# Performance work log

Measured on AMD Instinct MI355X. Metric: run time of the kernel, lower is better.

## Reference

```python
import jax, jax.numpy as jnp
import numpy as np

N, L, S = 2, 3000, 3000
C = 256          # in_depth
H = 256          # hidden_depth
FC = 8           # heads_count
SC_HID = H // FC # per-head dim of projected features
SCALE = (C // FC) ** 0.5  # torch code uses sc = in_depth // heads_count for scaling


def setup_inputs() -> dict:
    key = jax.random.key(0)
    ks = jax.random.split(key, 7)
    x0 = jax.random.normal(ks[0], (N, L, C), jnp.float32)
    x1 = jax.random.normal(ks[1], (N, S, C), jnp.float32)
    mask = jax.random.bernoulli(ks[2], 0.9, (N, L, S))
    W_proj = jax.random.normal(ks[3], (C, 2 * H), jnp.float32) / np.sqrt(C).astype(np.float32)
    b_proj = jax.random.normal(ks[4], (2 * H,), jnp.float32) * 0.01
    W_merge = jax.random.normal(ks[5], (H, C), jnp.float32) / np.sqrt(H).astype(np.float32)
    b_merge = jax.random.normal(ks[6], (C,), jnp.float32) * 0.01
    return {"x0": x0, "x1": x1, "mask": mask,
            "W_proj": W_proj, "b_proj": b_proj,
            "W_merge": W_merge, "b_merge": b_merge}


def _split_heads(x, W_proj, b_proj):
    # x: [n, t, C] -> proj [n, t, 2H] -> (qk, v) each [n, fc, t, sc]
    n, t, _ = x.shape
    p = (x @ W_proj + b_proj).reshape(n, t, 2, FC, SC_HID)  # layout (k fc sc)
    qk = jnp.transpose(p[:, :, 0], (0, 2, 1, 3))
    v = jnp.transpose(p[:, :, 1], (0, 2, 1, 3))
    return qk, v


def reference(x0, x1, mask, W_proj, b_proj, W_merge, b_merge):
    q0, v0 = _split_heads(x0, W_proj, b_proj)  # [n, f, l, d]
    q1, v1 = _split_heads(x1, W_proj, b_proj)  # [n, f, s, d]

    sim = jnp.einsum('nfld,nfsd->nfls', q0, q1)            # full score matrix
    sim = jnp.where(mask[:, None], sim, -jnp.inf) / SCALE  # mask then scale (as in torch)

    a01 = jnp.nan_to_num(jax.nn.softmax(sim, axis=3))  # rows over s
    a10 = jnp.nan_to_num(jax.nn.softmax(sim, axis=2))  # rows over l (== softmax(sim^T, -1))

    m0 = jnp.einsum('nfls,nfsd->nfld', a01, v1)  # [n, f, l, d]
    m1 = jnp.einsum('nfls,nfld->nfsd', a10, v0)  # [n, f, s, d]

    m0 = jnp.transpose(m0, (0, 2, 1, 3)).reshape(m0.shape[0], L, H) @ W_merge + b_merge
    m1 = jnp.transpose(m1, (0, 2, 1, 3)).reshape(m1.shape[0], S, H) @ W_merge + b_merge
    return m0, m1
```

## Files before the change

kernel.cpp:

```cpp
#include <hip/hip_runtime.h>
#include <cstdint>
#include <cstddef>

typedef unsigned int u32;
typedef unsigned short u16;
typedef uint8_t u8;
typedef unsigned long long u64;

constexpr int kNB = 2, kL = 3000, kS = 3000, kC = 256, kH = 256, kFC = 8, kD = 32;
constexpr int kTP = 3008;
constexpr int kMW = 48;
constexpr float kQSC = 0.5050097568f;

typedef __attribute__((ext_vector_type(8))) short short8;
typedef __attribute__((ext_vector_type(4))) float f32x4;

__device__ __forceinline__ u16 f2bf(float f) {
  u32 u = __float_as_uint(f);
  u += 0x7FFFu + ((u >> 16) & 1u);
  return (u16)(u >> 16);
}
__device__ __forceinline__ float bf2f(u16 h) { return __uint_as_float(((u32)h) << 16); }
__device__ __forceinline__ f32x4 mfma16(short8 a, short8 b, f32x4 c) {
  return __builtin_amdgcn_mfma_f32_16x16x32_bf16(a, b, c, 0, 0, 0);
}
__device__ __forceinline__ u32 pk2(float a, float b) {
  return (__float_as_uint(a) >> 16) | (__float_as_uint(b) & 0xFFFF0000u);
}
__device__ __forceinline__ u32 bytes_nz(u32 w) {
  return ((w & 0xFFu) ? 1u : 0u) | (((w >> 8) & 0xFFu) ? 2u : 0u)
       | (((w >> 16) & 0xFFu) ? 4u : 0u) | ((w >> 24) ? 8u : 0u);
}
__device__ __forceinline__ u32 h2_nz(u32 w) {
  return ((w & 0xFFFFu) ? 1u : 0u) | ((w >> 16) ? 2u : 0u);
}

constexpr size_t SZ_Q   = (size_t)kNB * kFC * kTP * kD * 2;
constexpr size_t SZ_MH  = (size_t)kNB * kTP * kH * 2;
constexpr size_t SZ_XB  = (size_t)kNB * kL * kC * 2;
constexpr size_t SZ_MKB = (size_t)kNB * kTP * kMW * 8;
constexpr size_t OFF_Q0 = 256;
constexpr size_t OFF_Q1 = OFF_Q0 + SZ_Q;
constexpr size_t OFF_V0 = OFF_Q1 + SZ_Q;
constexpr size_t OFF_V1 = OFF_V0 + SZ_Q;
constexpr size_t OFF_M0 = OFF_V1 + SZ_Q;
constexpr size_t OFF_M1 = OFF_M0 + SZ_MH;
constexpr size_t OFF_WT = OFF_M1 + SZ_MH;
constexpr size_t OFF_WM = OFF_WT + (size_t)2 * kH * kC * 2;
constexpr size_t OFF_X0 = OFF_WM + (size_t)kC * kH * 2;
constexpr size_t OFF_X1 = OFF_X0 + SZ_XB;
constexpr size_t OFF_MKB  = OFF_X1 + SZ_XB;
constexpr size_t OFF_MKBT = OFF_MKB + SZ_MKB;

__global__ __launch_bounds__(256) void k_detect(const u8* __restrict__ mraw,
                                                const u8* __restrict__ xraw,
                                                u32* __restrict__ flag) {
  __shared__ int c1[4], c3f[4], c3c, cexp;
  int tid = threadIdx.x;
  if (tid < 4) { c1[tid] = 0; c3f[tid] = 0; }
  if (tid == 0) { c3c = 0; cexp = 0; }
  __syncthreads();
  int l1[4] = {0,0,0,0}, l3f[4] = {0,0,0,0}, l3c = 0, lex = 0;
  for (int j = 0; j < 16; ++j) {
    int i = tid * 16 + j;
    u8 b = mraw[i];
    int r = i & 3;
    l1[r]  += (b == 1);
    l3f[r] += (b == 0x3F);
    if (i & 1) l3c += (b == 0x3C);
    if (r == 1) { u32 v = xraw[i] & 0x7F; lex += (v >= 0x3E && v <= 0x40); }
  }
  for (int r = 0; r < 4; ++r) {
    if (l1[r])  atomicAdd(&c1[r], l1[r]);
    if (l3f[r]) atomicAdd(&c3f[r], l3f[r]);
  }
  if (l3c) atomicAdd(&c3c, l3c);
  if (lex) atomicAdd(&cexp, lex);
  __syncthreads();
  if (tid == 0) {
    u32 mf;
    if (c1[1] + c1[2] + c1[3] > 64) mf = 0;
    else if (c1[0] > 64)            mf = 2;
    else if (c3f[1] > 64)           mf = 1;
    else if (c3c > 64)              mf = 4;
    else                            mf = 3;
    flag[0] = mf;
    flag[1] = (cexp > 300) ? 0u : 1u;
  }
}

constexpr int NB_MASK = 47 * 47 * 2;
constexpr int NB_CVT  = 3000;
constexpr int NB_WT   = 2 * kH + kC;

__global__ __launch_bounds__(256) void k_prep(const void* __restrict__ mraw,
                                              const void* __restrict__ x0,
                                              const void* __restrict__ x1,
                                              const void* __restrict__ Wp,
                                              const void* __restrict__ Wm,
                                              const u32* __restrict__ flag,
                                              u64* __restrict__ mkb, u64* __restrict__ mkbt,
                                              u16* __restrict__ xb0, u16* __restrict__ xb1,
                                              u16* __restrict__ WT, u16* __restrict__ WmT) {
  const int bx = blockIdx.x, tid = threadIdx.x;
  if (bx < NB_MASK) {
    const u32 mf = flag[0];
    const int n = bx / 2209, r2 = bx % 2209;
    const int l0 = (r2 / 47) * 64, s0 = (r2 % 47) * 64;
    __shared__ u16 tb[64][4];
    {
      const int row = tid >> 2, sg = (tid & 3) * 16;
      const int l = l0 + row;
      u32 bits = 0;
      if (l < kL) {
        const size_t base = ((size_t)n * kL + l) * kS + s0 + sg;
        const bool full = (s0 + sg + 16 <= kS);
        if (mf == 3) {
          if (full) {
            const float4* p = (const float4*)(((const float*)mraw) + base);
            float4 a = p[0], b = p[1], c = p[2], d = p[3];
            bits = (u32)(a.x != 0.f)        | ((u32)(a.y != 0.f) << 1)
                 | ((u32)(a.z != 0.f) << 2) | ((u32)(a.w != 0.f) << 3)
                 | ((u32)(b.x != 0.f) << 4) | ((u32)(b.y != 0.f) << 5)
                 | ((u32)(b.z != 0.f) << 6) | ((u32)(b.w != 0.f) << 7)
                 | ((u32)(c.x != 0.f) << 8) | ((u32)(c.y != 0.f) << 9)
                 | ((u32)(c.z != 0.f) << 10)| ((u32)(c.w != 0.f) << 11)
                 | ((u32)(d.x != 0.f) << 12)| ((u32)(d.y != 0.f) << 13)
                 | ((u32)(d.z != 0.f) << 14)| ((u32)(d.w != 0.f) << 15);
          } else {
            for (int i = 0; i < 16; ++i)
              if (s0 + sg + i < kS && ((const float*)mraw)[base + i] != 0.f) bits |= 1u << i;
          }
        } else if (mf == 2) {
          if (full) {
            const uint4* p = (const uint4*)(((const u32*)mraw) + base);
            uint4 a = p[0], b = p[1], c = p[2], d = p[3];
            bits = (u32)(a.x != 0)        | ((u32)(a.y != 0) << 1)
                 | ((u32)(a.z != 0) << 2) | ((u32)(a.w != 0) << 3)
                 | ((u32)(b.x != 0) << 4) | ((u32)(b.y != 0) << 5)
                 | ((u32)(b.z != 0) << 6) | ((u32)(b.w != 0) << 7)
                 | ((u32)(c.x != 0) << 8) | ((u32)(c.y != 0) << 9)
                 | ((u32)(c.z != 0) << 10)| ((u32)(c.w != 0) << 11)
                 | ((u32)(d.x != 0) << 12)| ((u32)(d.y != 0) << 13)
                 | ((u32)(d.z != 0) << 14)| ((u32)(d.w != 0) << 15);
          } else {
            for (int i = 0; i < 16; ++i)
              if (s0 + sg + i < kS && ((const u32*)mraw)[base + i]) bits |= 1u << i;
          }
        } else if (mf == 0) {
          if (full) {
            const u8* m8 = (const u8*)mraw + base;
            uint2 a = *(const uint2*)(m8);
            uint2 b = *(const uint2*)(m8 + 8);
            bits = bytes_nz(a.x) | (bytes_nz(a.y) << 4)
                 | (bytes_nz(b.x) << 8) | (bytes_nz(b.y) << 12);
          } else {
            for (int i = 0; i < 16; ++i)
              if (s0 + sg + i < kS && ((const u8*)mraw)[base + i]) bits |= 1u << i;
          }
        } else {
          if (full) {
            const u16* m16 = (const u16*)mraw + base;
            uint4 a = *(const uint4*)(m16);
            uint4 b = *(const uint4*)(m16 + 8);
            bits = h2_nz(a.x) | (h2_nz(a.y) << 2) | (h2_nz(a.z) << 4) | (h2_nz(a.w) << 6)
                 | (h2_nz(b.x) << 8) | (h2_nz(b.y) << 10)
                 | (h2_nz(b.z) << 12) | (h2_nz(b.w) << 14);
          } else {
            for (int i = 0; i < 16; ++i)
              if (s0 + sg + i < kS && ((const u16*)mraw)[base + i]) bits |= 1u << i;
          }
        }
      }
      tb[row][tid & 3] = (u16)bits;
    }
    __syncthreads();
    const int w = tid >> 6, lane = tid & 63;
    for (int k = 0; k < 16; ++k) {
      const int ro = w * 16 + k;
      u32 b1 = (tb[ro][lane >> 4] >> (lane & 15)) & 1;
      u64 word = __ballot((int)b1);
      if (lane == 0) mkb[((size_t)n * kTP + l0 + ro) * kMW + (s0 >> 6)] = word;
      u32 b2 = (tb[lane][ro >> 4] >> (ro & 15)) & 1;
      u64 wordt = __ballot((int)b2);
      if (lane == 0) mkbt[((size_t)n * kTP + s0 + ro) * kMW + (l0 >> 6)] = wordt;
    }
  } else if (bx < NB_MASK + NB_CVT) {
    const u32 f2 = flag[1];
    const int b2 = bx - NB_MASK;
    const void* X = (b2 >= 1500) ? x1 : x0;
    u16* B = (b2 >= 1500) ? xb1 : xb0;
    const int i = (b2 % 1500) * 256 + tid;
    if (f2 == 0) {
      ((uint2*)B)[i] = ((const uint2*)X)[i];
    } else {
      float4 v = ((const float4*)X)[i];
      uint2 o;
      o.x = (u32)f2bf(v.x) | ((u32)f2bf(v.y) << 16);
      o.y = (u32)f2bf(v.z) | ((u32)f2bf(v.w) << 16);
      ((uint2*)B)[i] = o;
    }
  } else {
    const u32 f2 = flag[1];
    const int b = bx - NB_MASK - NB_CVT, k = tid;
    if (b < 2 * kH) {
      int col = b;
      u16 v = (f2 == 0) ? ((const u16*)Wp)[(size_t)k * (2 * kH) + col]
                        : f2bf(((const float*)Wp)[(size_t)k * (2 * kH) + col]);
      WT[(size_t)col * kC + k] = v;
    } else {
      int col = b - 2 * kH;
      u16 v = (f2 == 0) ? ((const u16*)Wm)[(size_t)k * kC + col]
                        : f2bf(((const float*)Wm)[(size_t)k * kC + col]);
      WmT[(size_t)col * kH + k] = v;
    }
  }
}

__global__ __launch_bounds__(256) void k_proj(const u16* __restrict__ xb0,
                                              const u16* __restrict__ xb1,
                                              const u16* __restrict__ WT,
                                              const void* __restrict__ bias,
                                              const u32* __restrict__ flag,
                                              u16* __restrict__ q0, u16* __restrict__ v0t,
                                              u16* __restrict__ q1, u16* __restrict__ v1t) {
  const u32 f2 = flag[1];
  const int z = blockIdx.z;
  const u16* X = z ? xb1 : xb0;
  u16* Q = z ? q1 : q0;
  u16* V = z ? v1t : v0t;
  const int tid = threadIdx.x, w = tid >> 6, lane = tid & 63;
  const int quad = lane >> 4, c16 = lane & 15;
  const int rb = blockIdx.x, cb = blockIdx.y;

  __align__(16) __shared__ u16 sB[64 * 264];
  {
    const u16* wp = WT + (size_t)(cb * 64 + (tid >> 2)) * kC + (tid & 3) * 64;
    u16* sp = sB + (tid >> 2) * 264 + (tid & 3) * 64;
#pragma unroll
    for (int i = 0; i < 8; ++i) *(uint4*)(sp + i * 8) = *(const uint4*)(wp + i * 8);
  }
  __syncthreads();

  const int arow = rb * 64 + w * 16 + c16;
  const u16* ap = X + (size_t)arow * kC + quad * 8;
  f32x4 acc[4];
#pragma unroll
  for (int cg = 0; cg < 4; ++cg) acc[cg] = f32x4{0.f,0.f,0.f,0.f};
#pragma unroll
  for (int k0 = 0; k0 < 8; ++k0) {
    short8 a = *(const short8*)(ap + k0 * 32);
#pragma unroll
    for (int cg = 0; cg < 4; ++cg) {
      short8 b = *(const short8*)(sB + (cg * 16 + c16) * 264 + k0 * 32 + quad * 8);
      acc[cg] = mfma16(a, b, acc[cg]);
    }
  }

  const int row0 = rb * 64 + w * 16 + quad * 4;
  if (row0 < 6000) {
    const int n = (row0 >= kL) ? 1 : 0;
    const int t0 = row0 - n * kL;
#pragma unroll
    for (int cg = 0; cg < 4; ++cg) {
      const int c = cb * 64 + cg * 16 + c16;
      float bb = (f2 == 0) ? bf2f(((const u16*)bias)[c]) : ((const float*)bias)[c];
      if (c < kH) {
        int ff = c >> 5, d = c & 31;
        u16* qp = Q + ((size_t)(n * kFC + ff) * kTP + t0) * kD + d;
#pragma unroll
        for (int r = 0; r < 4; ++r) qp[(size_t)r * kD] = f2bf((acc[cg][r] + bb) * kQSC);
      } else {
        int cc = c - kH;
        int ff = cc >> 5, d = cc & 31;
        uint2 o;
        o.x = (u32)f2bf(acc[cg][0] + bb) | ((u32)f2bf(acc[cg][1] + bb) << 16);
        o.y = (u32)f2bf(acc[cg][2] + bb) | ((u32)f2bf(acc[cg][3] + bb) << 16);
        *(uint2*)(V + ((size_t)(n * kFC + ff) * kD + d) * kTP + t0) = o;
      }
    }
  }
}

__global__ __launch_bounds__(128, 1) void k_flash(const u16* __restrict__ q0,
                                                  const u16* __restrict__ q1,
                                                  const u16* __restrict__ v0t,
                                                  const u16* __restrict__ v1t,
                                                  const u64* __restrict__ mkb,
                                                  const u64* __restrict__ mkbt,
                                                  u16* __restrict__ m0h, u16* __restrict__ m1h) {
  const int z = blockIdx.z;
  const u16* QA = z ? q1 : q0;
  const u16* QB = z ? q0 : q1;
  const u16* VT = z ? v0t : v1t;
  const u64* MB = z ? mkbt : mkb;
  u16* MO = z ? m1h : m0h;

  const int nf = blockIdx.y, n = nf >> 3, f = nf & 7;
  const int tid = threadIdx.x, w = tid >> 6, lane = tid & 63;
  const int quad = lane >> 4, c16 = lane & 15;

  __align__(16) __shared__ float sBuf[8 * 9 * 64];
  u16* sP = (u16*)sBuf + w * 2 * (16 * 72);

  const u16* qa = QA + (size_t)(n * kFC + f) * kTP * kD;
  const u16* qb = QB + (size_t)(n * kFC + f) * kTP * kD;
  const u16* vt = VT + (size_t)(n * kFC + f) * kD * kTP;
  const u64* mb = MB + (size_t)n * kTP * kMW;

  const int l0 = blockIdx.x * 128;

  short8 af[8];
  int rc[8];
#pragma unroll
  for (int g = 0; g < 8; ++g) {
    int ra = l0 + g * 16 + c16;
    rc[g] = (ra > kTP - 1) ? (kTP - 1) : ra;
    af[g] = *(const short8*)(qa + (size_t)rc[g] * kD + quad * 8);
  }

  f32x4 acc[8][2];
  float pSum[8];
#pragma unroll
  for (int g = 0; g < 8; ++g) {
    acc[g][0] = f32x4{0.f,0.f,0.f,0.f};
    acc[g][1] = f32x4{0.f,0.f,0.f,0.f};
    pSum[g] = 0.f;
  }

  const int jc0 = w * 24;
  const int nch = w ? 23 : 24;
  uint4 mq[8];

#pragma unroll 1
  for (int jcl = 0; jcl < nch; ++jcl) {
    const int jc = jc0 + jcl;
    if ((jcl & 1) == 0) {
#pragma unroll
      for (int g = 0; g < 8; ++g)
        mq[g] = *(const uint4*)(mb + (size_t)rc[g] * kMW + jc);
    }
    const int j0 = jc * 64;
    const u16* qbase = qb + (size_t)(j0 + c16) * kD + quad * 8;
    short8 aq0 = *(const short8*)(qbase);
    short8 aq1 = *(const short8*)(qbase + (size_t)16 * kD);
    short8 aq2 = *(const short8*)(qbase + (size_t)32 * kD);
    short8 aq3 = *(const short8*)(qbase + (size_t)48 * kD);
    const u16* vb = vt + (size_t)c16 * kTP + j0 + quad * 8;
    short8 bv00 = *(const short8*)(vb);
    short8 bv01 = *(const short8*)(vb + (size_t)16 * kTP);
    short8 bv10 = *(const short8*)(vb + 32);
    short8 bv11 = *(const short8*)(vb + (size_t)16 * kTP + 32);

#pragma unroll
    for (int g = 0; g < 8; ++g) {
      const u32 lo = (jcl & 1) ? mq[g].z : mq[g].x;
      const u32 hi = (jcl & 1) ? mq[g].w : mq[g].y;
      u16* Pt = sP + (g & 1) * (16 * 72);
      float ps = 0.f;
#pragma unroll
      for (int t = 0; t < 4; ++t) {
        short8 aq = (t == 0) ? aq0 : (t == 1) ? aq1 : (t == 2) ? aq2 : aq3;
        f32x4 zz = {0.f,0.f,0.f,0.f};
        f32x4 s = mfma16(aq, af[g], zz);
        const u32 hh = (t & 2) ? hi : lo;
        const int base = (t & 1) * 16 + quad * 4;
        float p0 = ((hh >> (base + 0)) & 1) ? __builtin_amdgcn_exp2f(s[0]) : 0.f;
        float p1 = ((hh >> (base + 1)) & 1) ? __builtin_amdgcn_exp2f(s[1]) : 0.f;
        float p2 = ((hh >> (base + 2)) & 1) ? __builtin_amdgcn_exp2f(s[2]) : 0.f;
        float p3 = ((hh >> (base + 3)) & 1) ? __builtin_amdgcn_exp2f(s[3]) : 0.f;
        ps += (p0 + p1) + (p2 + p3);
        uint2 pw; pw.x = pk2(p0, p1); pw.y = pk2(p2, p3);
        *(uint2*)(Pt + c16 * 72 + t * 16 + quad * 4) = pw;
      }
      pSum[g] += ps;
      short8 ap0 = *(const short8*)(Pt + c16 * 72 + quad * 8);
      short8 ap1 = *(const short8*)(Pt + c16 * 72 + 32 + quad * 8);
      acc[g][0] = mfma16(ap0, bv00, acc[g][0]);
      acc[g][1] = mfma16(ap0, bv01, acc[g][1]);
      acc[g][0] = mfma16(ap1, bv10, acc[g][0]);
      acc[g][1] = mfma16(ap1, bv11, acc[g][1]);
    }
  }

#pragma unroll
  for (int g = 0; g < 8; ++g) {
    float s = pSum[g];
    s += __shfl_xor(s, 16);
    s += __shfl_xor(s, 32);
    pSum[g] = s;
  }

  __syncthreads();
  if (w == 1) {
#pragma unroll
    for (int g = 0; g < 8; ++g) {
#pragma unroll
      for (int r = 0; r < 4; ++r) {
        sBuf[(g * 9 + r)     * 64 + lane] = acc[g][0][r];
        sBuf[(g * 9 + 4 + r) * 64 + lane] = acc[g][1][r];
      }
      sBuf[(g * 9 + 8) * 64 + lane] = pSum[g];
    }
  }
  __syncthreads();
  if (w == 0) {
#pragma unroll
    for (int g = 0; g < 8; ++g) {
      float lsum = pSum[g] + sBuf[(g * 9 + 8) * 64 + lane];
#pragma unroll
      for (int r = 0; r < 4; ++r) {
        float n0 = acc[g][0][r] + sBuf[(g * 9 + r)     * 64 + lane];
        float n1 = acc[g][1][r] + sBuf[(g * 9 + 4 + r) * 64 + lane];
        float ls = __shfl(lsum, quad * 4 + r);
        float rd = (ls > 0.f) ? (1.f / ls) : 0.f;
        int lrow = l0 + g * 16 + quad * 4 + r;
        if (lrow < kL) {
          size_t basep = ((size_t)n * kTP + lrow) * kH + f * kD;
          MO[basep + c16]      = f2bf(n0 * rd);
          MO[basep + 16 + c16] = f2bf(n1 * rd);
        }
      }
    }
  }
}

__global__ __launch_bounds__(256) void k_merge(const u16* __restrict__ m0h,
                                               const u16* __restrict__ m1h,
                                               const u16* __restrict__ WmT,
                                               const void* __restrict__ bias,
                                               const u32* __restrict__ flag,
                                               void* __restrict__ out) {
  const u32 f2 = flag[1];
  const int z = blockIdx.z;
  const u16* A = z ? m1h : m0h;
  const int tid = threadIdx.x, w = tid >> 6, lane = tid & 63;
  const int quad = lane >> 4, c16 = lane & 15;
  const int rb = blockIdx.x, cb = blockIdx.y;

  __align__(16) __shared__ u16 sB[64 * 264];
  {
    const u16* wp = WmT + (size_t)(cb * 64 + (tid >> 2)) * kH + (tid & 3) * 64;
    u16* sp = sB + (tid >> 2) * 264 + (tid & 3) * 64;
#pragma unroll
    for (int i = 0; i < 8; ++i) *(uint4*)(sp + i * 8) = *(const uint4*)(wp + i * 8);
  }
  __syncthreads();

  const int arow = rb * 64 + w * 16 + c16;
  const u16* ap = A + (size_t)arow * kH + quad * 8;
  f32x4 acc[4];
#pragma unroll
  for (int cg = 0; cg < 4; ++cg) acc[cg] = f32x4{0.f,0.f,0.f,0.f};
#pragma unroll
  for (int k0 = 0; k0 < 8; ++k0) {
    short8 a = *(const short8*)(ap + k0 * 32);
#pragma unroll
    for (int cg = 0; cg < 4; ++cg) {
      short8 b = *(const short8*)(sB + (cg * 16 + c16) * 264 + k0 * 32 + quad * 8);
      acc[cg] = mfma16(a, b, acc[cg]);
    }
  }

  const int row0 = rb * 64 + w * 16 + quad * 4;
  const int n = (row0 >= kTP) ? 1 : 0;
  const int t0 = row0 - n * kTP;
  const size_t obase = (size_t)z * ((size_t)kNB * kL * kC);
#pragma unroll
  for (int cg = 0; cg < 4; ++cg) {
    const int c = cb * 64 + cg * 16 + c16;
    float bb = (f2 == 0) ? bf2f(((const u16*)bias)[c]) : ((const float*)bias)[c];
#pragma unroll
    for (int r = 0; r < 4; ++r) {
      const int t = t0 + r;
      if (t < kL) {
        size_t oi = obase + ((size_t)n * kL + t) * kC + c;
        float v = acc[cg][r] + bb;
        if (f2 == 0) ((u16*)out)[oi] = f2bf(v);
        else         ((float*)out)[oi] = v;
      }
    }
  }
}

extern "C" void kernel_launch(void* const* d_in, const int* in_sizes, int n_in,
                              void* d_out, int out_size, void* d_ws, size_t ws_size,
                              hipStream_t stream) {
  (void)in_sizes; (void)n_in; (void)out_size; (void)ws_size;
  u8* ws = (u8*)d_ws;
  u32* flag = (u32*)ws;
  u16* q0  = (u16*)(ws + OFF_Q0);
  u16* q1  = (u16*)(ws + OFF_Q1);
  u16* v0t = (u16*)(ws + OFF_V0);
  u16* v1t = (u16*)(ws + OFF_V1);
  u16* m0h = (u16*)(ws + OFF_M0);
  u16* m1h = (u16*)(ws + OFF_M1);
  u16* WT  = (u16*)(ws + OFF_WT);
  u16* WmT = (u16*)(ws + OFF_WM);
  u16* xb0 = (u16*)(ws + OFF_X0);
  u16* xb1 = (u16*)(ws + OFF_X1);
  u64* mkb  = (u64*)(ws + OFF_MKB);
  u64* mkbt = (u64*)(ws + OFF_MKBT);

  const void* x0 = d_in[0];
  const void* x1 = d_in[1];
  const void* mraw = d_in[2];
  const void* Wp = d_in[3];
  const void* bp = d_in[4];
  const void* Wm = d_in[5];
  const void* bm = d_in[6];

  k_detect<<<1, 256, 0, stream>>>((const u8*)mraw, (const u8*)x0, flag);
  k_prep<<<dim3(NB_MASK + NB_CVT + NB_WT), 256, 0, stream>>>(
      mraw, x0, x1, Wp, Wm, flag, mkb, mkbt, xb0, xb1, WT, WmT);
  k_proj<<<dim3(94, 8, 2), 256, 0, stream>>>(xb0, xb1, WT, bp, flag, q0, v0t, q1, v1t);
  k_flash<<<dim3(24, 16, 2), 128, 0, stream>>>(q0, q1, v0t, v1t, mkb, mkbt, m0h, m1h);
  k_merge<<<dim3(94, 4, 2), 256, 0, stream>>>(m0h, m1h, WmT, bm, flag, d_out);
}
```

Measured before the change: 303.8 us.

## Inline dtype detection into kernels and retile flash kernel to 4 warps, 64 rows

Removes the separate single-block detect kernel. Each block now recomputes the mask and input dtype flags from a small sample, which saves one launch and its serial dependency. The flash kernel moves from 128 threads over 128 query rows to 256 threads over 64 query rows. Its key chunks are split across 4 warps, the bitmask is stored column-major and fetched one word per lane with shuffles, and the 4 warp partials are reduced through shared memory. The row sum now uses bf16-truncated probabilities so it matches the values fed to the MFMA. In exchange, every block does redundant detection work with extra barriers, and the final reduction across warps grows.

New measurement: 255.2 us. -16.0%, faster.

```diff
diff --git a/kernel.cpp b/kernel.cpp
--- a/kernel.cpp
+++ b/kernel.cpp
@@ -27,6 +27,9 @@
 __device__ __forceinline__ u32 pk2(float a, float b) {
   return (__float_as_uint(a) >> 16) | (__float_as_uint(b) & 0xFFFF0000u);
 }
+__device__ __forceinline__ float truncbf(float a) {
+  return __uint_as_float(__float_as_uint(a) & 0xFFFF0000u);
+}
 __device__ __forceinline__ u32 bytes_nz(u32 w) {
   return ((w & 0xFFu) ? 1u : 0u) | (((w >> 8) & 0xFFu) ? 2u : 0u)
        | (((w >> 16) & 0xFFu) ? 4u : 0u) | ((w >> 24) ? 8u : 0u);
@@ -35,10 +38,60 @@
   return ((w & 0xFFFFu) ? 1u : 0u) | ((w >> 16) ? 2u : 0u);
 }
 
+__device__ __forceinline__ u32 detect_mf_block(const u8* __restrict__ mraw,
+                                               int tid, int* cnt) {
+  if (tid < 8) cnt[tid] = 0;
+  __syncthreads();
+  uint4 mv = ((const uint4*)mraw)[tid];
+  u32 wds[4] = {mv.x, mv.y, mv.z, mv.w};
+  int l1[4] = {0,0,0,0}; int l3f1 = 0, l3c = 0;
+#pragma unroll
+  for (int k = 0; k < 4; ++k) {
+    u32 wv = wds[k];
+#pragma unroll
+    for (int j = 0; j < 4; ++j) {
+      u32 b = (wv >> (8 * j)) & 0xFFu;
+      l1[j] += (b == 1u);
+      if (j == 1) l3f1 += (b == 0x3Fu);
+      if (j & 1) l3c += (b == 0x3Cu);
+    }
+  }
+  if (l1[0]) atomicAdd(&cnt[0], l1[0]);
+  if (l1[1]) atomicAdd(&cnt[1], l1[1]);
+  if (l1[2]) atomicAdd(&cnt[2], l1[2]);
+  if (l1[3]) atomicAdd(&cnt[3], l1[3]);
+  if (l3f1)  atomicAdd(&cnt[4], l3f1);
+  if (l3c)   atomicAdd(&cnt[5], l3c);
+  __syncthreads();
+  u32 mf;
+  if (cnt[1] + cnt[2] + cnt[3] > 64) mf = 0;
+  else if (cnt[0] > 64)              mf = 2;
+  else if (cnt[4] > 64)              mf = 1;
+  else if (cnt[5] > 64)              mf = 4;
+  else                               mf = 3;
+  return mf;
+}
+__device__ __forceinline__ u32 detect_f2_block(const u8* __restrict__ xraw,
+                                               int tid, int* cnt) {
+  if (tid == 0) cnt[0] = 0;
+  __syncthreads();
+  uint4 xv = ((const uint4*)xraw)[tid];
+  u32 wds[4] = {xv.x, xv.y, xv.z, xv.w};
+  int lex = 0;
+#pragma unroll
+  for (int k = 0; k < 4; ++k) {
+    u32 b = (wds[k] >> 8) & 0x7Fu;
+    lex += (b >= 0x3Eu && b <= 0x40u);
+  }
+  if (lex) atomicAdd(&cnt[0], lex);
+  __syncthreads();
+  return (cnt[0] > 300) ? 0u : 1u;
+}
+
 constexpr size_t SZ_Q   = (size_t)kNB * kFC * kTP * kD * 2;
 constexpr size_t SZ_MH  = (size_t)kNB * kTP * kH * 2;
 constexpr size_t SZ_XB  = (size_t)kNB * kL * kC * 2;
-constexpr size_t SZ_MKB = (size_t)kNB * kTP * kMW * 8;
+constexpr size_t SZ_MKB = (size_t)kNB * kMW * kTP * 8;
 constexpr size_t OFF_Q0 = 256;
 constexpr size_t OFF_Q1 = OFF_Q0 + SZ_Q;
 constexpr size_t OFF_V0 = OFF_Q1 + SZ_Q;
@@ -52,43 +105,6 @@
 constexpr size_t OFF_MKB  = OFF_X1 + SZ_XB;
 constexpr size_t OFF_MKBT = OFF_MKB + SZ_MKB;
 
-__global__ __launch_bounds__(256) void k_detect(const u8* __restrict__ mraw,
-                                                const u8* __restrict__ xraw,
-                                                u32* __restrict__ flag) {
-  __shared__ int c1[4], c3f[4], c3c, cexp;
-  int tid = threadIdx.x;
-  if (tid < 4) { c1[tid] = 0; c3f[tid] = 0; }
-  if (tid == 0) { c3c = 0; cexp = 0; }
-  __syncthreads();
-  int l1[4] = {0,0,0,0}, l3f[4] = {0,0,0,0}, l3c = 0, lex = 0;
-  for (int j = 0; j < 16; ++j) {
-    int i = tid * 16 + j;
-    u8 b = mraw[i];
-    int r = i & 3;
-    l1[r]  += (b == 1);
-    l3f[r] += (b == 0x3F);
-    if (i & 1) l3c += (b == 0x3C);
-    if (r == 1) { u32 v = xraw[i] & 0x7F; lex += (v >= 0x3E && v <= 0x40); }
-  }
-  for (int r = 0; r < 4; ++r) {
-    if (l1[r])  atomicAdd(&c1[r], l1[r]);
-    if (l3f[r]) atomicAdd(&c3f[r], l3f[r]);
-  }
-  if (l3c) atomicAdd(&c3c, l3c);
-  if (lex) atomicAdd(&cexp, lex);
-  __syncthreads();
-  if (tid == 0) {
-    u32 mf;
-    if (c1[1] + c1[2] + c1[3] > 64) mf = 0;
-    else if (c1[0] > 64)            mf = 2;
-    else if (c3f[1] > 64)           mf = 1;
-    else if (c3c > 64)              mf = 4;
-    else                            mf = 3;
-    flag[0] = mf;
-    flag[1] = (cexp > 300) ? 0u : 1u;
-  }
-}
-
 constexpr int NB_MASK = 47 * 47 * 2;
 constexpr int NB_CVT  = 3000;
 constexpr int NB_WT   = 2 * kH + kC;
@@ -98,13 +114,13 @@
                                               const void* __restrict__ x1,
                                               const void* __restrict__ Wp,
                                               const void* __restrict__ Wm,
-                                              const u32* __restrict__ flag,
                                               u64* __restrict__ mkb, u64* __restrict__ mkbt,
                                               u16* __restrict__ xb0, u16* __restrict__ xb1,
                                               u16* __restrict__ WT, u16* __restrict__ WmT) {
   const int bx = blockIdx.x, tid = threadIdx.x;
+  __shared__ int dcnt[8];
   if (bx < NB_MASK) {
-    const u32 mf = flag[0];
+    const u32 mf = detect_mf_block((const u8*)mraw, tid, dcnt);
     const int n = bx / 2209, r2 = bx % 2209;
     const int l0 = (r2 / 47) * 64, s0 = (r2 % 47) * 64;
     __shared__ u16 tb[64][4];
@@ -180,13 +196,13 @@
       const int ro = w * 16 + k;
       u32 b1 = (tb[ro][lane >> 4] >> (lane & 15)) & 1;
       u64 word = __ballot((int)b1);
-      if (lane == 0) mkb[((size_t)n * kTP + l0 + ro) * kMW + (s0 >> 6)] = word;
+      if (lane == 0) mkb[((size_t)n * kMW + (s0 >> 6)) * kTP + l0 + ro] = word;
       u32 b2 = (tb[lane][ro >> 4] >> (ro & 15)) & 1;
       u64 wordt = __ballot((int)b2);
-      if (lane == 0) mkbt[((size_t)n * kTP + s0 + ro) * kMW + (l0 >> 6)] = wordt;
+      if (lane == 0) mkbt[((size_t)n * kMW + (l0 >> 6)) * kTP + s0 + ro] = wordt;
     }
   } else if (bx < NB_MASK + NB_CVT) {
-    const u32 f2 = flag[1];
+    const u32 f2 = detect_f2_block((const u8*)x0, tid, dcnt);
     const int b2 = bx - NB_MASK;
     const void* X = (b2 >= 1500) ? x1 : x0;
     u16* B = (b2 >= 1500) ? xb1 : xb0;
@@ -201,7 +217,7 @@
       ((uint2*)B)[i] = o;
     }
   } else {
-    const u32 f2 = flag[1];
+    const u32 f2 = detect_f2_block((const u8*)x0, tid, dcnt);
     const int b = bx - NB_MASK - NB_CVT, k = tid;
     if (b < 2 * kH) {
       int col = b;
@@ -221,15 +237,17 @@
                                               const u16* __restrict__ xb1,
                                               const u16* __restrict__ WT,
                                               const void* __restrict__ bias,
-                                              const u32* __restrict__ flag,
+                                              const void* __restrict__ x0raw,
                                               u16* __restrict__ q0, u16* __restrict__ v0t,
                                               u16* __restrict__ q1, u16* __restrict__ v1t) {
-  const u32 f2 = flag[1];
+  __shared__ int dcnt[8];
+  const int tid = threadIdx.x;
+  const u32 f2 = detect_f2_block((const u8*)x0raw, tid, dcnt);
   const int z = blockIdx.z;
   const u16* X = z ? xb1 : xb0;
   u16* Q = z ? q1 : q0;
   u16* V = z ? v1t : v0t;
-  const int tid = threadIdx.x, w = tid >> 6, lane = tid & 63;
+  const int w = tid >> 6, lane = tid & 63;
   const int quad = lane >> 4, c16 = lane & 15;
   const int rb = blockIdx.x, cb = blockIdx.y;
 
@@ -282,13 +300,13 @@
   }
 }
 
-__global__ __launch_bounds__(128, 1) void k_flash(const u16* __restrict__ q0,
-                                                  const u16* __restrict__ q1,
-                                                  const u16* __restrict__ v0t,
-                                                  const u16* __restrict__ v1t,
-                                                  const u64* __restrict__ mkb,
-                                                  const u64* __restrict__ mkbt,
-                                                  u16* __restrict__ m0h, u16* __restrict__ m1h) {
+__global__ __launch_bounds__(256) void k_flash(const u16* __restrict__ q0,
+                                               const u16* __restrict__ q1,
+                                               const u16* __restrict__ v0t,
+                                               const u16* __restrict__ v1t,
+                                               const u64* __restrict__ mkb,
+                                               const u64* __restrict__ mkbt,
+                                               u16* __restrict__ m0h, u16* __restrict__ m1h) {
   const int z = blockIdx.z;
   const u16* QA = z ? q1 : q0;
   const u16* QB = z ? q0 : q1;
@@ -300,47 +318,36 @@
   const int tid = threadIdx.x, w = tid >> 6, lane = tid & 63;
   const int quad = lane >> 4, c16 = lane & 15;
 
-  __align__(16) __shared__ float sBuf[8 * 9 * 64];
-  u16* sP = (u16*)sBuf + w * 2 * (16 * 72);
+  __align__(16) __shared__ u16 sPall[4 * 4704];
+  u16* sP = sPall + w * 4704;
 
   const u16* qa = QA + (size_t)(n * kFC + f) * kTP * kD;
   const u16* qb = QB + (size_t)(n * kFC + f) * kTP * kD;
   const u16* vt = VT + (size_t)(n * kFC + f) * kD * kTP;
-  const u64* mb = MB + (size_t)n * kTP * kMW;
-
-  const int l0 = blockIdx.x * 128;
-
-  short8 af[8];
-  int rc[8];
-#pragma unroll
-  for (int g = 0; g < 8; ++g) {
-    int ra = l0 + g * 16 + c16;
-    rc[g] = (ra > kTP - 1) ? (kTP - 1) : ra;
-    af[g] = *(const short8*)(qa + (size_t)rc[g] * kD + quad * 8);
-  }
-
-  f32x4 acc[8][2];
-  float pSum[8];
-#pragma unroll
-  for (int g = 0; g < 8; ++g) {
+  const u64* mb = MB + (size_t)n * kMW * kTP;
+
+  const int l0 = blockIdx.x * 64;
+
+  short8 af[4];
+#pragma unroll
+  for (int g = 0; g < 4; ++g) {
+    const int ra = l0 + g * 16 + c16;
+    af[g] = *(const short8*)(qa + (size_t)ra * kD + quad * 8);
+  }
+
+  f32x4 acc[4][2];
+  float pSum[4];
+#pragma unroll
+  for (int g = 0; g < 4; ++g) {
     acc[g][0] = f32x4{0.f,0.f,0.f,0.f};
     acc[g][1] = f32x4{0.f,0.f,0.f,0.f};
     pSum[g] = 0.f;
   }
 
-  const int jc0 = w * 24;
-  const int nch = w ? 23 : 24;
-  uint4 mq[8];
-
 #pragma unroll 1
-  for (int jcl = 0; jcl < nch; ++jcl) {
-    const int jc = jc0 + jcl;
-    if ((jcl & 1) == 0) {
-#pragma unroll
-      for (int g = 0; g < 8; ++g)
-        mq[g] = *(const uint4*)(mb + (size_t)rc[g] * kMW + jc);
-    }
+  for (int jc = w; jc < 47; jc += 4) {
     const int j0 = jc * 64;
+    u64 mword = mb[(size_t)jc * kTP + l0 + lane];
     const u16* qbase = qb + (size_t)(j0 + c16) * kD + quad * 8;
     short8 aq0 = *(const short8*)(qbase);
     short8 aq1 = *(const short8*)(qbase + (size_t)16 * kD);
@@ -351,12 +358,12 @@
     short8 bv01 = *(const short8*)(vb + (size_t)16 * kTP);
     short8 bv10 = *(const short8*)(vb + 32);
     short8 bv11 = *(const short8*)(vb + (size_t)16 * kTP + 32);
-
-#pragma unroll
-    for (int g = 0; g < 8; ++g) {
-      const u32 lo = (jcl & 1) ? mq[g].z : mq[g].x;
-      const u32 hi = (jcl & 1) ? mq[g].w : mq[g].y;
-      u16* Pt = sP + (g & 1) * (16 * 72);
+    const u32 mlo = (u32)mword, mhi = (u32)(mword >> 32);
+
+#pragma unroll
+    for (int g = 0; g < 4; ++g) {
+      const u32 lo = (u32)__shfl((int)mlo, g * 16 + c16);
+      const u32 hi = (u32)__shfl((int)mhi, g * 16 + c16);
       float ps = 0.f;
 #pragma unroll
       for (int t = 0; t < 4; ++t) {
@@ -369,13 +376,13 @@
         float p1 = ((hh >> (base + 1)) & 1) ? __builtin_amdgcn_exp2f(s[1]) : 0.f;
         float p2 = ((hh >> (base + 2)) & 1) ? __builtin_amdgcn_exp2f(s[2]) : 0.f;
         float p3 = ((hh >> (base + 3)) & 1) ? __builtin_amdgcn_exp2f(s[3]) : 0.f;
-        ps += (p0 + p1) + (p2 + p3);
+        ps += (truncbf(p0) + truncbf(p1)) + (truncbf(p2) + truncbf(p3));
         uint2 pw; pw.x = pk2(p0, p1); pw.y = pk2(p2, p3);
-        *(uint2*)(Pt + c16 * 72 + t * 16 + quad * 4) = pw;
+        *(uint2*)(sP + (g * 16 + c16) * 72 + t * 16 + quad * 4) = pw;
       }
       pSum[g] += ps;
-      short8 ap0 = *(const short8*)(Pt + c16 * 72 + quad * 8);
-      short8 ap1 = *(const short8*)(Pt + c16 * 72 + 32 + quad * 8);
+      short8 ap0 = *(const short8*)(sP + (g * 16 + c16) * 72 + quad * 8);
+      short8 ap1 = *(const short8*)(sP + (g * 16 + c16) * 72 + 32 + quad * 8);
       acc[g][0] = mfma16(ap0, bv00, acc[g][0]);
       acc[g][1] = mfma16(ap0, bv01, acc[g][1]);
       acc[g][0] = mfma16(ap1, bv10, acc[g][0]);
@@ -384,7 +391,7 @@
   }
 
 #pragma unroll
-  for (int g = 0; g < 8; ++g) {
+  for (int g = 0; g < 4; ++g) {
     float s = pSum[g];
     s += __shfl_xor(s, 16);
     s += __shfl_xor(s, 32);
@@ -392,26 +399,34 @@
   }
 
   __syncthreads();
-  if (w == 1) {
-#pragma unroll
-    for (int g = 0; g < 8; ++g) {
+  float* buf = (float*)sPall;
+  if (w > 0) {
+    const int rbase = (w - 1) * 2304;
+#pragma unroll
+    for (int g = 0; g < 4; ++g) {
 #pragma unroll
       for (int r = 0; r < 4; ++r) {
-        sBuf[(g * 9 + r)     * 64 + lane] = acc[g][0][r];
-        sBuf[(g * 9 + 4 + r) * 64 + lane] = acc[g][1][r];
+        buf[rbase + (g * 9 + r)     * 64 + lane] = acc[g][0][r];
+        buf[rbase + (g * 9 + 4 + r) * 64 + lane] = acc[g][1][r];
       }
-      sBuf[(g * 9 + 8) * 64 + lane] = pSum[g];
+      buf[rbase + (g * 9 + 8) * 64 + lane] = pSum[g];
     }
   }
   __syncthreads();
   if (w == 0) {
 #pragma unroll
-    for (int g = 0; g < 8; ++g) {
-      float lsum = pSum[g] + sBuf[(g * 9 + 8) * 64 + lane];
+    for (int g = 0; g < 4; ++g) {
+      float lsum = pSum[g];
+#pragma unroll
+      for (int ww = 0; ww < 3; ++ww) lsum += buf[ww * 2304 + (g * 9 + 8) * 64 + lane];
 #pragma unroll
       for (int r = 0; r < 4; ++r) {
-        float n0 = acc[g][0][r] + sBuf[(g * 9 + r)     * 64 + lane];
-        float n1 = acc[g][1][r] + sBuf[(g * 9 + 4 + r) * 64 + lane];
+        float n0 = acc[g][0][r], n1 = acc[g][1][r];
+#pragma unroll
+        for (int ww = 0; ww < 3; ++ww) {
+          n0 += buf[ww * 2304 + (g * 9 + r)     * 64 + lane];
+          n1 += buf[ww * 2304 + (g * 9 + 4 + r) * 64 + lane];
+        }
         float ls = __shfl(lsum, quad * 4 + r);
         float rd = (ls > 0.f) ? (1.f / ls) : 0.f;
         int lrow = l0 + g * 16 + quad * 4 + r;
@@ -429,12 +444,14 @@
                                                const u16* __restrict__ m1h,
                                                const u16* __restrict__ WmT,
                                                const void* __restrict__ bias,
-                                               const u32* __restrict__ flag,
+                                               const void* __restrict__ x0raw,
                                                void* __restrict__ out) {
-  const u32 f2 = flag[1];
+  __shared__ int dcnt[8];
+  const int tid = threadIdx.x;
+  const u32 f2 = detect_f2_block((const u8*)x0raw, tid, dcnt);
   const int z = blockIdx.z;
   const u16* A = z ? m1h : m0h;
-  const int tid = threadIdx.x, w = tid >> 6, lane = tid & 63;
+  const int w = tid >> 6, lane = tid & 63;
   const int quad = lane >> 4, c16 = lane & 15;
   const int rb = blockIdx.x, cb = blockIdx.y;
 
@@ -488,7 +505,6 @@
                               hipStream_t stream) {
   (void)in_sizes; (void)n_in; (void)out_size; (void)ws_size;
   u8* ws = (u8*)d_ws;
-  u32* flag = (u32*)ws;
   u16* q0  = (u16*)(ws + OFF_Q0);
   u16* q1  = (u16*)(ws + OFF_Q1);
   u16* v0t = (u16*)(ws + OFF_V0);
@@ -510,10 +526,9 @@
   const void* Wm = d_in[5];
   const void* bm = d_in[6];
 
-  k_detect<<<1, 256, 0, stream>>>((const u8*)mraw, (const u8*)x0, flag);
   k_prep<<<dim3(NB_MASK + NB_CVT + NB_WT), 256, 0, stream>>>(
-      mraw, x0, x1, Wp, Wm, flag, mkb, mkbt, xb0, xb1, WT, WmT);
-  k_proj<<<dim3(94, 8, 2), 256, 0, stream>>>(xb0, xb1, WT, bp, flag, q0, v0t, q1, v1t);
-  k_flash<<<dim3(24, 16, 2), 128, 0, stream>>>(q0, q1, v0t, v1t, mkb, mkbt, m0h, m1h);
-  k_merge<<<dim3(94, 4, 2), 256, 0, stream>>>(m0h, m1h, WmT, bm, flag, d_out);
-}
+      mraw, x0, x1, Wp, Wm, mkb, mkbt, xb0, xb1, WT, WmT);
+  k_proj<<<dim3(94, 8, 2), 256, 0, stream>>>(xb0, xb1, WT, bp, x0, q0, v0t, q1, v1t);
+  k_flash<<<dim3(47, 16, 2), 256, 0, stream>>>(q0, q1, v0t, v1t, mkb, mkbt, m0h, m1h);
+  k_merge<<<dim3(94, 4, 2), 256, 0, stream>>>(m0h, m1h, WmT, bm, x0, d_out);
+}
```
